# Optimization experiments

Hardware: AMD Instinct MI355X
Metric: run time of the kernel (lower is better)

Reference implementation:

```python
import jax, jax.numpy as jnp
import numpy as np


def setup_inputs() -> dict:
    key = jax.random.key(0)
    ks = jax.random.split(key, 8)
    B, C, H, W = 4, 512, 64, 64
    C8 = C // 8
    return {
        "x": jax.random.normal(ks[0], (B, C, H, W), dtype=jnp.float32),
        "Wq": jax.random.normal(ks[1], (C8, C), dtype=jnp.float32) * 0.02,
        "bq": jax.random.normal(ks[2], (C8,), dtype=jnp.float32) * 0.02,
        "Wk": jax.random.normal(ks[3], (C8, C), dtype=jnp.float32) * 0.02,
        "bk": jax.random.normal(ks[4], (C8,), dtype=jnp.float32) * 0.02,
        "Wv": jax.random.normal(ks[5], (C, C), dtype=jnp.float32) * 0.02,
        "bv": jax.random.normal(ks[6], (C,), dtype=jnp.float32) * 0.02,
        "gamma": jax.random.normal(ks[7], (1,), dtype=jnp.float32),
    }


def reference(x, Wq, bq, Wk, bk, Wv, bv, gamma):
    B, C, H, W = x.shape
    N = H * W
    xf = x.reshape(B, C, N)  # 1x1 conv == per-position matmul over channels
    q = jnp.einsum('oc,bcn->bno', Wq, xf) + bq  # B, N, C//8  (proj_query^T)
    k = jnp.einsum('oc,bcn->bon', Wk, xf) + bk[None, :, None]  # B, C//8, N
    v = jnp.einsum('oc,bcn->bon', Wv, xf) + bv[None, :, None]  # B, C, N
    energy = jnp.einsum('bno,bom->bnm', q, k)  # B, N, N
    attention = jax.nn.softmax(energy, axis=-1)
    # out = bmm(proj_value, attention^T): out[:, :, n] = sum_m v[:, :, m] * att[n, m]
    out = jnp.einsum('bcm,bnm->bcn', v, attention).reshape(B, C, H, W)
    return gamma[0] * out + x
```

## Files before the change

kernel.cpp:

```cpp
#include <hip/hip_runtime.h>
#include <stdint.h>


typedef unsigned short u16;
typedef unsigned char u8;
typedef __attribute__((ext_vector_type(8))) short short8;
typedef __attribute__((ext_vector_type(4))) float f32x4;
typedef __attribute__((ext_vector_type(16))) float f32x16;
typedef __attribute__((ext_vector_type(4))) int i32x4;
typedef __attribute__((ext_vector_type(8))) int i32x8;

#define ASYNC16(gp, lp)                                                        \
  __builtin_amdgcn_global_load_lds(                                            \
      (__attribute__((address_space(1))) void*)(void*)(gp),                    \
      (__attribute__((address_space(3))) void*)(lp), 16, 0, 0)

#define WAIT_VM0 0x0F70
#define WAIT_VM4 0x0F74
#define WAIT_VM8 0x0F78

#define EXP_SHIFT 5.0f
#define EXP_CAP 57000.0f

__device__ __forceinline__ u16 f2bf(float f) {
  uint32_t u = __float_as_uint(f);
  u += 0x7FFFu + ((u >> 16) & 1u);
  return (u16)(u >> 16);
}

__device__ __forceinline__ u8 f2fp8(float f) {
  f = fminf(fmaxf(f, -440.f), 440.f);
  int r = __builtin_amdgcn_cvt_pk_fp8_f32(f, f, 0, false);
  return (u8)(r & 0xFF);
}

__global__ __launch_bounds__(256) void k_transpose(const float* __restrict__ x,
                                                   u16* __restrict__ xT) {
  __shared__ float tile[32][33];
  const int b = blockIdx.z;
  const int nb = blockIdx.x * 32;
  const int cb = blockIdx.y * 32;
  const int t = threadIdx.x;
  {
    const int nl = t & 31, c0 = t >> 5;
    const float* xp = x + ((size_t)b * 512 + cb) * 4096 + nb;
#pragma unroll
    for (int i = 0; i < 4; ++i) {
      const int cl = c0 + i * 8;
      tile[cl][nl] = xp[(size_t)cl * 4096 + nl];
    }
  }
  __syncthreads();
  {
    const int cl = t & 31, n0 = t >> 5;
    u16* xtp = xT + ((size_t)b * 4096 + nb) * 512 + cb;
#pragma unroll
    for (int i = 0; i < 4; ++i) {
      const int nl = n0 + i * 8;
      xtp[(size_t)nl * 512 + cl] = f2bf(tile[cl][nl]);
    }
  }
}

__global__ __launch_bounds__(256) void k_wcast(const float* __restrict__ Wq,
                                               const float* __restrict__ Wk,
                                               const float* __restrict__ Wv,
                                               u16* __restrict__ wqk,
                                               u16* __restrict__ wv) {
  const int idx = blockIdx.x * 256 + threadIdx.x;
  if (idx < 128 * 512) {
    const int r = idx >> 9, c = idx & 511;
    const float f = (r < 64) ? Wq[r * 512 + c] : Wk[(r - 64) * 512 + c];
    wqk[idx] = f2bf(f);
  } else {
    const int j = idx - 128 * 512;
    if (j < 512 * 512) wv[j] = f2bf(Wv[j]);
  }
}

__device__ __forceinline__ void gemm_bt_tile(const u16* __restrict__ A,
                                             const u16* __restrict__ B,
                                             const int K, const int rowA0,
                                             const int colB0, u16* smem,
                                             f32x4 acc[4][4]) {
  const int t = threadIdx.x;
  const int lane = t & 63, wave = t >> 6;
  const int quad = lane >> 4, l15 = lane & 15;
  const int wr = wave >> 1, wc = wave & 1;
  u16* As = smem;
  u16* Bs = smem + 8192;
  const f32x4 zero = {0.f, 0.f, 0.f, 0.f};
#pragma unroll
  for (int i = 0; i < 4; ++i)
#pragma unroll
    for (int j = 0; j < 4; ++j) acc[i][j] = zero;

  const int srow = t >> 3;
  const int c8 = (lane & 7) ^ (lane >> 3);
  const u16* ga = A + (size_t)(rowA0 + srow) * K + c8 * 8;
  const u16* gb = B + (size_t)(colB0 + srow) * K + c8 * 8;
  char* la = (char*)As + wave * 1024;
  char* lb = (char*)Bs + wave * 1024;
  const size_t rK32 = (size_t)32 * K;

  const int sw0 = (quad) ^ (l15 & 7);
  const int sw1 = (4 + quad) ^ (l15 & 7);

  for (int k0 = 0; k0 < K; k0 += 64) {
    ASYNC16(ga + k0, la);
    ASYNC16(ga + k0 + rK32, la + 4096);
    ASYNC16(ga + k0 + 2 * rK32, la + 8192);
    ASYNC16(ga + k0 + 3 * rK32, la + 12288);
    ASYNC16(gb + k0, lb);
    ASYNC16(gb + k0 + rK32, lb + 4096);
    ASYNC16(gb + k0 + 2 * rK32, lb + 8192);
    ASYNC16(gb + k0 + 3 * rK32, lb + 12288);
    __syncthreads();
#pragma unroll
    for (int s = 0; s < 2; ++s) {
      const int sw = s ? sw1 : sw0;
      short8 a[4], b[4];
#pragma unroll
      for (int i = 0; i < 4; ++i)
        a[i] = *(const short8*)(As + (wr * 64 + i * 16 + l15) * 64 + sw * 8);
#pragma unroll
      for (int j = 0; j < 4; ++j)
        b[j] = *(const short8*)(Bs + (wc * 64 + j * 16 + l15) * 64 + sw * 8);
#pragma unroll
      for (int i = 0; i < 4; ++i)
#pragma unroll
        for (int j = 0; j < 4; ++j)
          acc[i][j] = __builtin_amdgcn_mfma_f32_16x16x32_bf16(a[i], b[j],
                                                              acc[i][j], 0, 0, 0);
    }
    __syncthreads();
  }
}

__global__ __launch_bounds__(256) void k_proj_qk(const u16* __restrict__ xT,
                                                 const u16* __restrict__ wqk,
                                                 const float* __restrict__ bq,
                                                 const float* __restrict__ bk,
                                                 u16* __restrict__ q,
                                                 u16* __restrict__ kT) {
  __shared__ u16 smem[16384];
  const int b = blockIdx.z;
  const int rowA0 = blockIdx.x * 128;
  f32x4 acc[4][4];
  gemm_bt_tile(xT + (size_t)b * 4096 * 512, wqk, 512, rowA0, 0, smem, acc);
  const int t = threadIdx.x, lane = t & 63, wave = t >> 6;
  const int quad = lane >> 4, l15 = lane & 15;
  const int wr = wave >> 1, wc = wave & 1;
#pragma unroll
  for (int j = 0; j < 4; ++j) {
    const int col = wc * 64 + j * 16 + l15;
    const float bias = (col < 64) ? bq[col] : bk[col - 64];
#pragma unroll
    for (int i = 0; i < 4; ++i) {
#pragma unroll
      for (int r = 0; r < 4; ++r) {
        const int row = rowA0 + wr * 64 + i * 16 + quad * 4 + r;
        const float val = acc[i][j][r] + bias;
        if (col < 64)
          q[((size_t)b * 4096 + row) * 64 + col] = f2bf(val);
        else
          kT[((size_t)b * 4096 + row) * 64 + (col - 64)] = f2bf(val);
      }
    }
  }
}

__global__ __launch_bounds__(256) void k_proj_v(const u16* __restrict__ wv,
                                                const u16* __restrict__ xT,
                                                const float* __restrict__ bv,
                                                u8* __restrict__ v8) {
  __shared__ u16 smem[16384];
  const int b = blockIdx.z;
  const int rowA0 = blockIdx.x * 128;
  const int colB0 = blockIdx.y * 128;
  f32x4 acc[4][4];
  gemm_bt_tile(wv, xT + (size_t)b * 4096 * 512, 512, rowA0, colB0, smem, acc);
  const int t = threadIdx.x, lane = t & 63, wave = t >> 6;
  const int quad = lane >> 4, l15 = lane & 15;
  const int wr = wave >> 1, wc = wave & 1;
#pragma unroll
  for (int i = 0; i < 4; ++i) {
#pragma unroll
    for (int r = 0; r < 4; ++r) {
      const int row = rowA0 + wr * 64 + i * 16 + quad * 4 + r;
      const float bias = bv[row];
#pragma unroll
      for (int j = 0; j < 4; ++j) {
        const int col = colB0 + wc * 64 + j * 16 + l15;
        v8[((size_t)b * 512 + row) * 4096 + col] = f2fp8(acc[i][j][r] + bias);
      }
    }
  }
}

__global__ __launch_bounds__(256, 4) void k_attn(const u16* __restrict__ q,
                                                 const u16* __restrict__ kT,
                                                 u8* __restrict__ E8,
                                                 float* __restrict__ lpart) {
  __shared__ u16 qs[4][16 * 64];
  __shared__ u16 ks[2][128 * 64];

  const int t = threadIdx.x;
  const int l = t & 63;
  const int w = t >> 6;
  const int quad = l >> 4, l15 = l & 15;
  const int c8 = (l & 7) ^ (l >> 3);
  const int r8 = l >> 3;

  const int row0 = blockIdx.x * 64 + w * 16;
  const int mpart = blockIdx.y;
  const int b = blockIdx.z;
  const int m_base = mpart * 1024;

  const u16* qg = q + ((size_t)b * 4096 + row0) * 64 + (size_t)r8 * 64 + c8 * 8;
  const u16* kg = kT + ((size_t)b * 4096 + m_base + w * 32) * 64 +
                  (size_t)r8 * 64 + c8 * 8;

  char* qls = (char*)qs + w * 2048;
  char* kls0 = (char*)ks[0] + w * 4096;
  char* kls1 = (char*)ks[1] + w * 4096;

  ASYNC16(qg, qls);
  ASYNC16(qg + 512, qls + 1024);
#pragma unroll
  for (int i = 0; i < 4; ++i) ASYNC16(kg + i * 512, kls0 + i * 1024);
#pragma unroll
  for (int i = 0; i < 4; ++i) ASYNC16(kg + 8192 + i * 512, kls1 + i * 1024);

  __builtin_amdgcn_s_waitcnt(WAIT_VM8);

  const int sw0 = quad ^ (l15 & 7);
  const int sw1 = (4 + quad) ^ (l15 & 7);
  const u16* qsw = qs[w];
  const short8 af0 = *(const short8*)(qsw + l15 * 64 + sw0 * 8);
  const short8 af1 = *(const short8*)(qsw + l15 * 64 + sw1 * 8);

  float lsum = 0.f;
  u8* Ep = E8 + ((size_t)b * 4096 + row0 + l15) * 4096 + m_base + quad * 4;
  const f32x4 zero = {0.f, 0.f, 0.f, 0.f};

  for (int it = 0; it < 8; ++it) {
    if (it < 7)
      __builtin_amdgcn_s_waitcnt(WAIT_VM4);
    else
      __builtin_amdgcn_s_waitcnt(WAIT_VM0);
    __builtin_amdgcn_s_barrier();
    asm volatile("" ::: "memory");

    const u16* kb = ks[it & 1];
    f32x4 acc[8];
#pragma unroll
    for (int j = 0; j < 8; ++j) acc[j] = zero;
#pragma unroll
    for (int j = 0; j < 8; ++j)
      acc[j] = __builtin_amdgcn_mfma_f32_16x16x32_bf16(
          *(const short8*)(kb + (j * 16 + l15) * 64 + sw0 * 8), af0, acc[j], 0, 0, 0);
#pragma unroll
    for (int j = 0; j < 8; ++j)
      acc[j] = __builtin_amdgcn_mfma_f32_16x16x32_bf16(
          *(const short8*)(kb + (j * 16 + l15) * 64 + sw1 * 8), af1, acc[j], 0, 0, 0);
#pragma unroll
    for (int j = 0; j < 8; ++j) {
      const float e0 = fminf(__expf(acc[j][0] - EXP_SHIFT), EXP_CAP);
      const float e1 = fminf(__expf(acc[j][1] - EXP_SHIFT), EXP_CAP);
      const float e2 = fminf(__expf(acc[j][2] - EXP_SHIFT), EXP_CAP);
      const float e3 = fminf(__expf(acc[j][3] - EXP_SHIFT), EXP_CAP);
      lsum += (e0 + e1) + (e2 + e3);
      int pk = __builtin_amdgcn_cvt_pk_bf8_f32(e0, e1, 0, false);
      pk = __builtin_amdgcn_cvt_pk_bf8_f32(e2, e3, pk, true);
      *(int*)(Ep + it * 128 + j * 16) = pk;
    }

    asm volatile("" ::: "memory");
    __builtin_amdgcn_s_barrier();
    if (it < 6) {
      char* dst = (it & 1) ? kls1 : kls0;
      const u16* src = kg + (size_t)(it + 2) * 8192;
#pragma unroll
      for (int i = 0; i < 4; ++i) ASYNC16(src + i * 512, dst + i * 1024);
    }
  }

  lsum += __shfl_xor(lsum, 16);
  lsum += __shfl_xor(lsum, 32);
  if (l < 16)
    lpart[(size_t)mpart * 16384 + (size_t)b * 4096 + row0 + l] = lsum;
}

__global__ __launch_bounds__(256) void k_lsum(const float* __restrict__ lp,
                                              float* __restrict__ ilg) {
  const int i = blockIdx.x * 256 + threadIdx.x;
  ilg[i] = 1.0f / (lp[i] + lp[16384 + i] + lp[32768 + i] + lp[49152 + i]);
}

__global__ __launch_bounds__(256) void k_pv(const u8* __restrict__ v8,
                                            const u8* __restrict__ E8,
                                            const float* __restrict__ ilg,
                                            const float* __restrict__ x,
                                            const float* __restrict__ gamma,
                                            float* __restrict__ out) {
  __shared__ u8 As[8192];
  __shared__ u8 Bs[8192];
  const int bid = blockIdx.x;
  const int xcd = bid & 7;
  const int slot = bid >> 3;
  const int c_idx = slot >> 4;
  const int group = xcd * 16 + (slot & 15);
  const int b = group >> 5;
  const int n_idx = group & 31;
  const int rowA0 = c_idx * 128;
  const int colB0 = n_idx * 128;

  const u8* Ag = v8 + (size_t)b * 512 * 4096;
  const u8* Bg = E8 + (size_t)b * 4096 * 4096;

  const int t = threadIdx.x;
  const int l = t & 63, w = t >> 6;
  const int wr = w >> 1, wc = w & 1;
  const int l31 = l & 31, h = l >> 5;

  const int srow = w * 16 + (l >> 2);
  const int ca = l & 3;
  const int f0 = (srow >> 1) & 3;
  const int f1 = ((srow + 64) >> 1) & 3;
  const u8* gA0 = Ag + (size_t)(rowA0 + srow) * 4096 + (ca ^ f0) * 16;
  const u8* gA1 = Ag + (size_t)(rowA0 + srow + 64) * 4096 + (ca ^ f1) * 16;
  const u8* gB0 = Bg + (size_t)(colB0 + srow) * 4096 + (ca ^ f0) * 16;
  const u8* gB1 = Bg + (size_t)(colB0 + srow + 64) * 4096 + (ca ^ f1) * 16;
  char* la = (char*)As + w * 1024;
  char* lb = (char*)Bs + w * 1024;

  int rowA[2], rowB[2], sA1[2], sA2[2], sB1[2], sB2[2];
#pragma unroll
  for (int i = 0; i < 2; ++i) {
    rowA[i] = wr * 64 + i * 32 + l31;
    const int fa = (rowA[i] >> 1) & 3;
    sA1[i] = (2 * h) ^ fa;
    sA2[i] = (2 * h + 1) ^ fa;
    rowB[i] = wc * 64 + i * 32 + l31;
    const int fb = (rowB[i] >> 1) & 3;
    sB1[i] = (2 * h) ^ fb;
    sB2[i] = (2 * h + 1) ^ fb;
  }

  f32x16 acc[2][2];
#pragma unroll
  for (int i = 0; i < 2; ++i)
#pragma unroll
    for (int j = 0; j < 2; ++j)
#pragma unroll
      for (int r = 0; r < 16; ++r) acc[i][j][r] = 0.f;

  for (int k0 = 0; k0 < 4096; k0 += 64) {
    ASYNC16(gA0 + k0, la);
    ASYNC16(gA1 + k0, la + 4096);
    ASYNC16(gB0 + k0, lb);
    ASYNC16(gB1 + k0, lb + 4096);
    __syncthreads();
    i32x8 a[2], bb[2];
#pragma unroll
    for (int i = 0; i < 2; ++i) {
      const u8* pa = As + rowA[i] * 64;
      const i32x4 lo = *(const i32x4*)(pa + sA1[i] * 16);
      const i32x4 hi = *(const i32x4*)(pa + sA2[i] * 16);
      a[i][0] = lo[0]; a[i][1] = lo[1]; a[i][2] = lo[2]; a[i][3] = lo[3];
      a[i][4] = hi[0]; a[i][5] = hi[1]; a[i][6] = hi[2]; a[i][7] = hi[3];
      const u8* pb = Bs + rowB[i] * 64;
      const i32x4 blo = *(const i32x4*)(pb + sB1[i] * 16);
      const i32x4 bhi = *(const i32x4*)(pb + sB2[i] * 16);
      bb[i][0] = blo[0]; bb[i][1] = blo[1]; bb[i][2] = blo[2]; bb[i][3] = blo[3];
      bb[i][4] = bhi[0]; bb[i][5] = bhi[1]; bb[i][6] = bhi[2]; bb[i][7] = bhi[3];
    }
#pragma unroll
    for (int i = 0; i < 2; ++i)
#pragma unroll
      for (int j = 0; j < 2; ++j)
        acc[i][j] = __builtin_amdgcn_mfma_scale_f32_32x32x64_f8f6f4(
            a[i], bb[j], acc[i][j], 0 , 1 , 0, 0x7F, 0, 0x7F);
    __syncthreads();
  }

  const float g = gamma[0];
#pragma unroll
  for (int j = 0; j < 2; ++j) {
    const int col = colB0 + wc * 64 + j * 32 + l31;
    const float gil = g * ilg[(size_t)b * 4096 + col];
#pragma unroll
    for (int i = 0; i < 2; ++i) {
#pragma unroll
      for (int r = 0; r < 16; ++r) {
        const int rloc = (r & 3) + 8 * (r >> 2) + 4 * h;
        const int row = rowA0 + wr * 64 + i * 32 + rloc;
        const size_t idx = ((size_t)b * 512 + row) * 4096 + col;
        out[idx] = gil * acc[i][j][r] + x[idx];
      }
    }
  }
}

extern "C" void kernel_launch(void* const* d_in, const int* in_sizes, int n_in,
                              void* d_out, int out_size, void* d_ws,
                              size_t ws_size, hipStream_t stream) {
  const float* x = (const float*)d_in[0];
  const float* Wq = (const float*)d_in[1];
  const float* bq = (const float*)d_in[2];
  const float* Wk = (const float*)d_in[3];
  const float* bk = (const float*)d_in[4];
  const float* Wv = (const float*)d_in[5];
  const float* bv = (const float*)d_in[6];
  const float* gamma = (const float*)d_in[7];
  float* out = (float*)d_out;

  char* ws = (char*)d_ws;
  u16* xT = (u16*)(ws);
  u16* wqk = (u16*)(ws + 16777216);
  u16* wv = (u16*)(ws + 16908288);
  u16* qb = (u16*)(ws + 17432576);
  u16* ktb = (u16*)(ws + 19529728);
  u8* v8 = (u8*)(ws + 21626880);
  u8* E8 = (u8*)(ws + 30015488);
  float* lpart = (float*)(ws + 97124352);
  float* ilg = (float*)(ws + 97386496);

  k_transpose<<<dim3(128, 16, 4), 256, 0, stream>>>(x, xT);
  k_wcast<<<dim3(1280), 256, 0, stream>>>(Wq, Wk, Wv, wqk, wv);
  k_proj_qk<<<dim3(32, 1, 4), 256, 0, stream>>>(xT, wqk, bq, bk, qb, ktb);
  k_proj_v<<<dim3(4, 32, 4), 256, 0, stream>>>(wv, xT, bv, v8);
  k_attn<<<dim3(64, 4, 4), 256, 0, stream>>>(qb, ktb, E8, lpart);
  k_lsum<<<dim3(64), 256, 0, stream>>>(lpart, ilg);
  k_pv<<<dim3(512), 256, 0, stream>>>(v8, E8, ilg, x, gamma, out);
}
```

Before: 212.9 us.

## Multi-buffer PV kernel LDS with async prefetch two stages ahead

The PV matmul kernel moves from a single LDS buffer, loaded and consumed with two barriers per k-step, to a 4-slot ring. Loads are issued two iterations ahead and gated by vmcnt waits, so one barrier per iteration suffices and global loads overlap MFMA work. s_setprio is raised around MFMA blocks in both the energy and PV kernels to favour math-issuing waves. LDS use grows from 16KB to 64KB per block, which may reduce occupancy.

```diff
diff --git a/kernel.cpp b/kernel.cpp
--- a/kernel.cpp
+++ b/kernel.cpp
@@ -256,6 +256,7 @@
     f32x4 acc[8];
 #pragma unroll
     for (int j = 0; j < 8; ++j) acc[j] = zero;
+    __builtin_amdgcn_s_setprio(1);
 #pragma unroll
     for (int j = 0; j < 8; ++j)
       acc[j] = __builtin_amdgcn_mfma_f32_16x16x32_bf16(
@@ -264,6 +265,7 @@
     for (int j = 0; j < 8; ++j)
       acc[j] = __builtin_amdgcn_mfma_f32_16x16x32_bf16(
           *(const short8*)(kb + (j * 16 + l15) * 64 + sw1 * 8), af1, acc[j], 0, 0, 0);
+    __builtin_amdgcn_s_setprio(0);
 #pragma unroll
     for (int j = 0; j < 8; ++j) {
       const float e0 = fminf(__expf(acc[j][0] - EXP_SHIFT), EXP_CAP);
@@ -304,8 +306,8 @@
                                             const float* __restrict__ x,
                                             const float* __restrict__ gamma,
                                             float* __restrict__ out) {
-  __shared__ u8 As[8192];
-  __shared__ u8 Bs[8192];
+  __shared__ u8 As[4][8192];
+  __shared__ u8 Bs[4][8192];
   const int bid = blockIdx.x;
   const int xcd = bid & 7;
   const int slot = bid >> 3;
@@ -332,8 +334,16 @@
   const u8* gA1 = Ag + (size_t)(rowA0 + srow + 64) * 4096 + (ca ^ f1) * 16;
   const u8* gB0 = Bg + (size_t)(colB0 + srow) * 4096 + (ca ^ f0) * 16;
   const u8* gB1 = Bg + (size_t)(colB0 + srow + 64) * 4096 + (ca ^ f1) * 16;
-  char* la = (char*)As + w * 1024;
-  char* lb = (char*)Bs + w * 1024;
+
+#define STAGE_PV(bi, k0)                                                       \
+  do {                                                                         \
+    char* la_ = (char*)As[bi] + w * 1024;                                      \
+    char* lb_ = (char*)Bs[bi] + w * 1024;                                      \
+    ASYNC16(gA0 + (k0), la_);                                                  \
+    ASYNC16(gA1 + (k0), la_ + 4096);                                           \
+    ASYNC16(gB0 + (k0), lb_);                                                  \
+    ASYNC16(gB1 + (k0), lb_ + 4096);                                           \
+  } while (0)
 
   int rowA[2], rowB[2], sA1[2], sA2[2], sB1[2], sB2[2];
 #pragma unroll
@@ -356,34 +366,46 @@
 #pragma unroll
       for (int r = 0; r < 16; ++r) acc[i][j][r] = 0.f;
 
-  for (int k0 = 0; k0 < 4096; k0 += 64) {
-    ASYNC16(gA0 + k0, la);
-    ASYNC16(gA1 + k0, la + 4096);
-    ASYNC16(gB0 + k0, lb);
-    ASYNC16(gB1 + k0, lb + 4096);
-    __syncthreads();
+  STAGE_PV(0, 0);
+  STAGE_PV(1, 64);
+
+  for (int it = 0; it < 64; ++it) {
+    if (it < 63)
+      __builtin_amdgcn_s_waitcnt(WAIT_VM4);
+    else
+      __builtin_amdgcn_s_waitcnt(WAIT_VM0);
+    asm volatile("" ::: "memory");
+    __builtin_amdgcn_s_barrier();
+    asm volatile("" ::: "memory");
+    if (it + 2 < 64) STAGE_PV((it + 2) & 3, (it + 2) * 64);
+
+    const u8* Asb = As[it & 3];
+    const u8* Bsb = Bs[it & 3];
     i32x8 a[2], bb[2];
 #pragma unroll
     for (int i = 0; i < 2; ++i) {
-      const u8* pa = As + rowA[i] * 64;
+      const u8* pa = Asb + rowA[i] * 64;
       const i32x4 lo = *(const i32x4*)(pa + sA1[i] * 16);
       const i32x4 hi = *(const i32x4*)(pa + sA2[i] * 16);
       a[i][0] = lo[0]; a[i][1] = lo[1]; a[i][2] = lo[2]; a[i][3] = lo[3];
       a[i][4] = hi[0]; a[i][5] = hi[1]; a[i][6] = hi[2]; a[i][7] = hi[3];
-      const u8* pb = Bs + rowB[i] * 64;
+      const u8* pb = Bsb + rowB[i] * 64;
       const i32x4 blo = *(const i32x4*)(pb + sB1[i] * 16);
       const i32x4 bhi = *(const i32x4*)(pb + sB2[i] * 16);
       bb[i][0] = blo[0]; bb[i][1] = blo[1]; bb[i][2] = blo[2]; bb[i][3] = blo[3];
       bb[i][4] = bhi[0]; bb[i][5] = bhi[1]; bb[i][6] = bhi[2]; bb[i][7] = bhi[3];
     }
+    __builtin_amdgcn_s_setprio(1);
 #pragma unroll
     for (int i = 0; i < 2; ++i)
 #pragma unroll
       for (int j = 0; j < 2; ++j)
         acc[i][j] = __builtin_amdgcn_mfma_scale_f32_32x32x64_f8f6f4(
             a[i], bb[j], acc[i][j], 0 , 1 , 0, 0x7F, 0, 0x7F);
-    __syncthreads();
-  }
+    __builtin_amdgcn_s_setprio(0);
+    asm volatile("" ::: "memory");
+  }
+#undef STAGE_PV
 
   const float g = gamma[0];
 #pragma unroll
```

Measured after the change: 213.2 us. About the same (+0.1%).
